# Optimization experiments

Hardware: AMD Instinct MI355X
Metric: run time of the kernel (lower is better)

## Reference

```python
import jax, jax.numpy as jnp
import numpy as np

EPS = 1e-3  # keras BatchNormalization default epsilon
K = 16


def _graph_feature(x, k):
    # x: [B, N, C] -> edge: [B, N, k, 2C]
    sq = jnp.sum(x * x, axis=-1)                       # [B, N]
    # negative squared distance (larger = closer); self is max
    pd = 2.0 * jnp.einsum('bnc,bmc->bnm', x, x) - sq[:, :, None] - sq[:, None, :]
    _, idx = jax.lax.top_k(pd, k)                      # [B, N, k]
    nbr = jax.vmap(lambda xb, ib: xb[ib])(x, idx)      # [B, N, k, C]
    ctr = jnp.broadcast_to(x[:, :, None, :], nbr.shape)
    return jnp.concatenate([ctr, nbr], axis=-1)        # [B, N, k, 2C]


def _bn(y, g, b, m, v):
    return (y - m) * (g * jax.lax.rsqrt(v + EPS)) + b


def _edge_block(x, W, g, b, m, v, k):
    e = _graph_feature(x, k)                           # [B, N, k, 2C]
    h = jnp.einsum('bnkc,cd->bnkd', e, W)              # 1x1 conv, no bias
    h = jax.nn.relu(_bn(h, g, b, m, v))
    return jnp.max(h, axis=2)                          # [B, N, D]


def setup_inputs() -> dict:
    key = jax.random.key(0)
    ks = jax.random.split(key, 32)
    B, N = 8, 2048
    x = jax.random.normal(ks[0], (B, N, 3), dtype=jnp.float32)
    dims = [(6, 64), (128, 64), (128, 128), (256, 256), (512, 512)]
    d = {'x': x}
    for i, (cin, cout) in enumerate(dims):
        j = i + 1
        d[f'W{j}'] = jax.random.normal(ks[1 + i], (cin, cout), dtype=jnp.float32) * (1.0 / np.sqrt(cin))
        d[f'g{j}'] = jax.random.uniform(ks[6 + i], (cout,), dtype=jnp.float32, minval=0.5, maxval=1.5)
        d[f'b{j}'] = jax.random.normal(ks[11 + i], (cout,), dtype=jnp.float32) * 0.1
        d[f'm{j}'] = jax.random.normal(ks[16 + i], (cout,), dtype=jnp.float32) * 0.1
        d[f'v{j}'] = jax.random.uniform(ks[21 + i], (cout,), dtype=jnp.float32, minval=0.5, maxval=1.5)
    return d


def reference(x, W1, g1, b1, m1, v1, W2, g2, b2, m2, v2, W3, g3, b3, m3, v3,
              W4, g4, b4, m4, v4, W5, g5, b5, m5, v5):
    x1 = _edge_block(x,  W1, g1, b1, m1, v1, K)   # [B, N, 64]
    x2 = _edge_block(x1, W2, g2, b2, m2, v2, K)   # [B, N, 64]
    x3 = _edge_block(x2, W3, g3, b3, m3, v3, K)   # [B, N, 128]
    x4 = _edge_block(x3, W4, g4, b4, m4, v4, K)   # [B, N, 256]
    x5 = jnp.concatenate([x1, x2, x3, x4], axis=-1)  # [B, N, 512]
    h5 = jnp.einsum('bnc,cd->bnd', x5, W5)           # 1x1 conv1d, no bias
    return jax.nn.relu(_bn(h5, g5, b5, m5, v5))      # [B, N, 512]
```

## Files before the change

kernel.cpp:

```cpp
#include <hip/hip_runtime.h>

#define NP 2048
#define BTOT 8
#define BN_TOT 16384
#define KC 16
#define NTILE 32
#define NEG_INF (-__builtin_inff())

typedef __attribute__((ext_vector_type(8))) short short8;
typedef __attribute__((ext_vector_type(4))) float f32x4;

__device__ __forceinline__ unsigned short bf16_rne(float x) {
  unsigned u = __float_as_uint(x);
  u += 0x7FFFu + ((u >> 16) & 1u);
  return (unsigned short)(u >> 16);
}
__device__ __forceinline__ void split2(float x, unsigned short& h, unsigned short& l) {
  h = bf16_rne(x);
  float hf = __uint_as_float((unsigned)h << 16);
  l = bf16_rne(x - hf);
}

template <typename JM>
__device__ __forceinline__ void select16(const float (&v)[32], int lane, float* svw,
                                         int* sjw, int* out, int jb, JM jmap) {
  float lmax = v[0];
#pragma unroll
  for (int t = 1; t < 32; ++t) lmax = fmaxf(lmax, v[t]);
  int rank = 0;
  for (int s = 0; s < 64; ++s) {
    float o = __shfl(lmax, s, 64);
    rank += (o > lmax) || (o == lmax && s < lane);
  }
  unsigned long long m15 = __ballot(rank == 15);
  float T0 = __shfl(lmax, (int)__builtin_ctzll(m15), 64);

  unsigned long long lowmask = (1ull << lane) - 1ull;
  unsigned keepmask = 0u;
  int base = 0;
#pragma unroll
  for (int t = 0; t < 32; ++t) {
    bool keep = (v[t] >= T0);
    unsigned long long mk = __ballot(keep);
    if (keep) {
      keepmask |= (1u << t);
      int pos = base + (int)__popcll(mk & lowmask);
      if (pos < 256) { svw[pos] = v[t]; sjw[pos] = jmap(t); }
    }
    base += (int)__popcll(mk);
  }
  int cnt = base;

  if (cnt <= 64) {
    __threadfence_block();
    float mv = NEG_INF;
    int mj = 1 << 30;
    if (lane < cnt) { mv = svw[lane]; mj = sjw[lane]; }
    int rk = 0;
    for (int s = 0; s < 64; ++s) {
      float ov = __shfl(mv, s, 64);
      int oj = __shfl(mj, s, 64);
      rk += (ov > mv) || (ov == mv && oj < mj);
    }
    if (lane < cnt && rk < 16) out[rk] = jb + mj;
    return;
  }

  if (cnt <= 256) {
    __threadfence_block();
    for (int r = 0; r < 16; ++r) {
      float lbv = NEG_INF;
      int lbj = 1 << 30, lbp = -1;
      for (int i = lane; i < cnt; i += 64) {
        float cv = svw[i];
        int cj = sjw[i];
        if (cv > lbv || (cv == lbv && cj < lbj)) { lbv = cv; lbj = cj; lbp = i; }
      }
      float bv = lbv;
      int bj = lbj;
#pragma unroll
      for (int off = 32; off > 0; off >>= 1) {
        float ov = __shfl_xor(bv, off, 64);
        int oj = __shfl_xor(bj, off, 64);
        if (ov > bv || (ov == bv && oj < bj)) { bv = ov; bj = oj; }
      }
      if (lane == 0) out[r] = jb + bj;
      if (lbp >= 0 && lbj == bj) svw[lbp] = NEG_INF;
      __threadfence_block();
    }
    return;
  }

  {
    unsigned avail = keepmask;
    for (int r = 0; r < 16; ++r) {
      float bv = NEG_INF;
      int bj = 1 << 30, bt = -1;
      unsigned am = avail;
      while (am) {
        int t = __builtin_ctz(am);
        am &= am - 1;
        float vv = v[t];
        int jj = jmap(t);
        if (vv > bv || (vv == bv && jj < bj)) { bv = vv; bj = jj; bt = t; }
      }
      float gv = bv;
      int gj = bj;
#pragma unroll
      for (int off = 32; off > 0; off >>= 1) {
        float ov = __shfl_xor(gv, off, 64);
        int oj = __shfl_xor(gj, off, 64);
        if (ov > gv || (ov == gv && oj < gj)) { gv = ov; gj = oj; }
      }
      if (lane == 0) out[r] = jb + gj;
      if (bt >= 0 && bj == gj) avail &= ~(1u << bt);
    }
  }
}

__global__ __launch_bounds__(256) void sqnorm_kernel(const float* __restrict__ X,
                                                     int lda, int C,
                                                     float* __restrict__ sq) {
  int wave = threadIdx.x >> 6, lane = threadIdx.x & 63;
  int row = blockIdx.x * 4 + wave;
  float s = 0.f;
  for (int c = lane; c < C; c += 64) {
    float t = X[(size_t)row * lda + c];
    s += t * t;
  }
#pragma unroll
  for (int off = 32; off > 0; off >>= 1) s += __shfl_xor(s, off, 64);
  if (lane == 0) sq[row] = s;
}

__global__ __launch_bounds__(256) void dist_gemm(const float* __restrict__ X, int lda, int K,
                                                 const float* __restrict__ sq,
                                                 float* __restrict__ pd, int batch0) {
  int bz = blockIdx.z;
  const float* Xb = X + (size_t)(batch0 + bz) * NP * lda;
  const float* sqb = sq + (size_t)(batch0 + bz) * NP;
  float* pdb = pd + (size_t)bz * NP * NP;
  int rem = blockIdx.x, bi = 0;
  while (rem >= NTILE - bi) { rem -= NTILE - bi; ++bi; }
  int bj = bi + rem;
  int i0 = bi * 64, j0 = bj * 64;
  __shared__ float At[KC][68];
  __shared__ float Bt[KC][68];
  int t = threadIdx.x;
  int tx = t & 15, ty = t >> 4;
  int lk = t & 15, lr = t >> 4;
  float acc[4][4] = {};
  for (int k0 = 0; k0 < K; k0 += KC) {
    int kk = k0 + lk;
    bool kv = kk < K;
#pragma unroll
    for (int u = 0; u < 4; ++u) {
      int r = lr + u * 16;
      At[lk][r] = kv ? Xb[(size_t)(i0 + r) * lda + kk] : 0.f;
      Bt[lk][r] = kv ? Xb[(size_t)(j0 + r) * lda + kk] : 0.f;
    }
    __syncthreads();
#pragma unroll
    for (int q = 0; q < KC; ++q) {
      float4 a4 = *(const float4*)&At[q][ty * 4];
      float4 b4 = *(const float4*)&Bt[q][tx * 4];
      float a[4] = {a4.x, a4.y, a4.z, a4.w};
      float bv[4] = {b4.x, b4.y, b4.z, b4.w};
#pragma unroll
      for (int ii = 0; ii < 4; ++ii)
#pragma unroll
        for (int jj = 0; jj < 4; ++jj)
          acc[ii][jj] = fmaf(a[ii], bv[jj], acc[ii][jj]);
    }
    __syncthreads();
  }
  float4 sqj4 = *(const float4*)&sqb[j0 + tx * 4];
#pragma unroll
  for (int ii = 0; ii < 4; ++ii) {
    int i = i0 + ty * 4 + ii;
    float4 o;
    o.x = 2.f * acc[ii][0] - sqj4.x;
    o.y = 2.f * acc[ii][1] - sqj4.y;
    o.z = 2.f * acc[ii][2] - sqj4.z;
    o.w = 2.f * acc[ii][3] - sqj4.w;
    *(float4*)&pdb[(size_t)i * NP + j0 + tx * 4] = o;
  }
  if (bi != bj) {
    float4 sqi4 = *(const float4*)&sqb[i0 + ty * 4];
#pragma unroll
    for (int jj = 0; jj < 4; ++jj) {
      int j = j0 + tx * 4 + jj;
      float4 o;
      o.x = 2.f * acc[0][jj] - sqi4.x;
      o.y = 2.f * acc[1][jj] - sqi4.y;
      o.z = 2.f * acc[2][jj] - sqi4.z;
      o.w = 2.f * acc[3][jj] - sqi4.w;
      *(float4*)&pdb[(size_t)j * NP + i0 + ty * 4] = o;
    }
  }
}

__global__ __launch_bounds__(256) void topk_kernel(const float* __restrict__ pd,
                                                   int* __restrict__ idx_out, int batch0) {
  __shared__ float sv[4][256];
  __shared__ int sj[4][256];
  int wave = threadIdx.x >> 6, lane = threadIdx.x & 63;
  int row = blockIdx.x * 4 + wave;
  const float* prow = pd + (size_t)row * NP;
  int grow = batch0 * NP + row;
  int jb = (grow >> 11) << 11;
  float v[32];
#pragma unroll
  for (int u = 0; u < 8; ++u) {
    float4 q = *(const float4*)&prow[u * 256 + (lane << 2)];
    v[u * 4 + 0] = q.x;
    v[u * 4 + 1] = q.y;
    v[u * 4 + 2] = q.z;
    v[u * 4 + 3] = q.w;
  }
  select16(v, lane, sv[wave], sj[wave], idx_out + (size_t)grow * 16, jb,
           [lane](int t) { return ((t >> 2) << 8) + (lane << 2) + (t & 3); });
}

__global__ __launch_bounds__(256) void dist3_topk(const float* __restrict__ x,
                                                  int* __restrict__ idx_out) {
  __shared__ float4 xs4[NP];
  __shared__ float sv[4][256];
  __shared__ int sj[4][256];
  int wave = threadIdx.x >> 6, lane = threadIdx.x & 63;
  int b = blockIdx.x >> 7;
  int row0 = (blockIdx.x & 127) * 16;
  const float* xb = x + (size_t)b * NP * 3;
  for (int n = threadIdx.x; n < NP; n += 256) {
    float a0 = xb[3 * n], a1 = xb[3 * n + 1], a2 = xb[3 * n + 2];
    xs4[n] = make_float4(a0, a1, a2, a0 * a0 + a1 * a1 + a2 * a2);
  }
  __syncthreads();
  int jb = b << 11;
  for (int rr = 0; rr < 4; ++rr) {
    int row = row0 + wave * 4 + rr;
    float4 c = xs4[row];
    float v[32];
#pragma unroll
    for (int t = 0; t < 32; ++t) {
      int j = lane + t * 64;
      float4 p = xs4[j];
      float dot = c.x * p.x + c.y * p.y + c.z * p.z;
      v[t] = 2.f * dot - p.w;
    }
    select16(v, lane, sv[wave], sj[wave], idx_out + (size_t)(jb + row) * 16, jb,
             [lane](int t) { return lane + t * 64; });
  }
}

__global__ __launch_bounds__(256) void feat_gemm(const float* __restrict__ A, int lda, int K,
                                                 const float* __restrict__ W, int D,
                                                 float* __restrict__ outT,
                                                 float* __restrict__ outB) {
  const float* Wz = W + (size_t)blockIdx.z * K * D;
  float* o = blockIdx.z ? outB : outT;
  int n0 = blockIdx.x * 64, m0 = blockIdx.y * 64;
  __shared__ float At[KC][68];
  __shared__ float Bt[KC][68];
  int t = threadIdx.x;
  int tx = t & 15, ty = t >> 4;
  float acc[4][4] = {};
  for (int k0 = 0; k0 < K; k0 += KC) {
    {
      int lk = t & 15, lr = t >> 4;
      int kk = k0 + lk;
      bool kv = kk < K;
#pragma unroll
      for (int u = 0; u < 4; ++u) {
        int r = lr + u * 16;
        At[lk][r] = kv ? A[(size_t)(m0 + r) * lda + kk] : 0.f;
      }
      int n = t & 63, kq0 = t >> 6;
#pragma unroll
      for (int u = 0; u < 4; ++u) {
        int kq = kq0 + u * 4;
        int kg = k0 + kq;
        Bt[kq][n] = (kg < K) ? Wz[(size_t)kg * D + n0 + n] : 0.f;
      }
    }
    __syncthreads();
#pragma unroll
    for (int q = 0; q < KC; ++q) {
      float4 a4 = *(const float4*)&At[q][ty * 4];
      float4 b4 = *(const float4*)&Bt[q][tx * 4];
      float a[4] = {a4.x, a4.y, a4.z, a4.w};
      float bv[4] = {b4.x, b4.y, b4.z, b4.w};
#pragma unroll
      for (int ii = 0; ii < 4; ++ii)
#pragma unroll
        for (int jj = 0; jj < 4; ++jj)
          acc[ii][jj] = fmaf(a[ii], bv[jj], acc[ii][jj]);
    }
    __syncthreads();
  }
#pragma unroll
  for (int ii = 0; ii < 4; ++ii) {
    float4 o4 = make_float4(acc[ii][0], acc[ii][1], acc[ii][2], acc[ii][3]);
    *(float4*)&o[(size_t)(m0 + ty * 4 + ii) * D + n0 + tx * 4] = o4;
  }
}

__global__ __launch_bounds__(256) void gather_bn_relu(const float* __restrict__ ZT,
                                                      const float* __restrict__ YB,
                                                      const int* __restrict__ idx, int D,
                                                      const float* __restrict__ g,
                                                      const float* __restrict__ bta,
                                                      const float* __restrict__ mu,
                                                      const float* __restrict__ va,
                                                      float* __restrict__ X5, int coff) {
  __shared__ int nb[16];
  int bn = blockIdx.x, d = threadIdx.x;
  if (d < 16) nb[d] = idx[(size_t)bn * 16 + d];
  __syncthreads();
  float mx = NEG_INF;
#pragma unroll
  for (int j = 0; j < 16; ++j) mx = fmaxf(mx, YB[(size_t)nb[j] * D + d]);
  float h = ZT[(size_t)bn * D + d] + mx;
  float s = g[d] / sqrtf(va[d] + 1e-3f);
  float val = (h - mu[d]) * s + bta[d];
  X5[(size_t)bn * 512 + coff + d] = fmaxf(val, 0.f);
}

__global__ __launch_bounds__(256) void split_x5(const float* __restrict__ X5,
                                                unsigned short* __restrict__ Xh,
                                                unsigned short* __restrict__ Xl) {
  const int total4 = BN_TOT * 512 / 4;
  for (int i = blockIdx.x * 256 + threadIdx.x; i < total4; i += gridDim.x * 256) {
    float4 v = *(const float4*)&X5[i * 4];
    ushort4 h, l;
    split2(v.x, h.x, l.x);
    split2(v.y, h.y, l.y);
    split2(v.z, h.z, l.z);
    split2(v.w, h.w, l.w);
    *(ushort4*)&Xh[i * 4] = h;
    *(ushort4*)&Xl[i * 4] = l;
  }
}

__global__ __launch_bounds__(256) void w5t_split(const float* __restrict__ W5,
                                                 unsigned short* __restrict__ Wh,
                                                 unsigned short* __restrict__ Wl) {
  int n = blockIdx.x;
  for (int k = threadIdx.x; k < 512; k += 256) {
    unsigned short h, l;
    split2(W5[(size_t)k * 512 + n], h, l);
    Wh[(size_t)n * 512 + k] = h;
    Wl[(size_t)n * 512 + k] = l;
  }
}

__global__ __launch_bounds__(256) void final_mfma(const unsigned short* __restrict__ Ah,
                                                  const unsigned short* __restrict__ Al,
                                                  const unsigned short* __restrict__ Bh,
                                                  const unsigned short* __restrict__ Bl,
                                                  const float* __restrict__ g,
                                                  const float* __restrict__ bta,
                                                  const float* __restrict__ mu,
                                                  const float* __restrict__ va,
                                                  float* __restrict__ out) {
  int tid = threadIdx.x;
  int wave = tid >> 6, lane = tid & 63;
  int wm = wave >> 1, wn = wave & 1;
  int ln = lane & 15, quad = lane >> 4;
  int m_base = blockIdx.y * 128 + wm * 64;
  int n_base = blockIdx.x * 128 + wn * 64;

  f32x4 acc[4][4];
#pragma unroll
  for (int i = 0; i < 4; ++i)
#pragma unroll
    for (int j = 0; j < 4; ++j) acc[i][j] = (f32x4){0.f, 0.f, 0.f, 0.f};

  size_t aoff[4], boff[4];
#pragma unroll
  for (int t = 0; t < 4; ++t) {
    aoff[t] = (size_t)(m_base + t * 16 + ln) * 512 + quad * 8;
    boff[t] = (size_t)(n_base + t * 16 + ln) * 512 + quad * 8;
  }

  short8 cAh[4], cAl[4], cBh[4], cBl[4];
#pragma unroll
  for (int t = 0; t < 4; ++t) {
    cAh[t] = *(const short8*)(Ah + aoff[t]);
    cAl[t] = *(const short8*)(Al + aoff[t]);
    cBh[t] = *(const short8*)(Bh + boff[t]);
    cBl[t] = *(const short8*)(Bl + boff[t]);
  }

  for (int kk = 0; kk < 16; ++kk) {
    short8 nAh[4], nAl[4], nBh[4], nBl[4];
    if (kk < 15) {
      int ko = (kk + 1) * 32;
#pragma unroll
      for (int t = 0; t < 4; ++t) {
        nAh[t] = *(const short8*)(Ah + aoff[t] + ko);
        nAl[t] = *(const short8*)(Al + aoff[t] + ko);
        nBh[t] = *(const short8*)(Bh + boff[t] + ko);
        nBl[t] = *(const short8*)(Bl + boff[t] + ko);
      }
    }
#pragma unroll
    for (int tm = 0; tm < 4; ++tm)
#pragma unroll
      for (int tn = 0; tn < 4; ++tn) {
        acc[tm][tn] = __builtin_amdgcn_mfma_f32_16x16x32_bf16(cAh[tm], cBh[tn],
                                                              acc[tm][tn], 0, 0, 0);
        acc[tm][tn] = __builtin_amdgcn_mfma_f32_16x16x32_bf16(cAh[tm], cBl[tn],
                                                              acc[tm][tn], 0, 0, 0);
        acc[tm][tn] = __builtin_amdgcn_mfma_f32_16x16x32_bf16(cAl[tm], cBh[tn],
                                                              acc[tm][tn], 0, 0, 0);
      }
    if (kk < 15) {
#pragma unroll
      for (int t = 0; t < 4; ++t) {
        cAh[t] = nAh[t];
        cAl[t] = nAl[t];
        cBh[t] = nBh[t];
        cBl[t] = nBl[t];
      }
    }
  }

#pragma unroll
  for (int tn = 0; tn < 4; ++tn) {
    int col = n_base + tn * 16 + ln;
    float s = g[col] / sqrtf(va[col] + 1e-3f);
    float tc = bta[col] - mu[col] * s;
#pragma unroll
    for (int tm = 0; tm < 4; ++tm) {
      int mrow = m_base + tm * 16 + quad * 4;
#pragma unroll
      for (int r = 0; r < 4; ++r) {
        float val = acc[tm][tn][r] * s + tc;
        out[(size_t)(mrow + r) * 512 + col] = fmaxf(val, 0.f);
      }
    }
  }
}

extern "C" void kernel_launch(void* const* d_in, const int* in_sizes, int n_in,
                              void* d_out, int out_size, void* d_ws, size_t ws_size,
                              hipStream_t stream) {
  const float* x = (const float*)d_in[0];
  const float *W[5], *g[5], *bt[5], *mu[5], *va[5];
  for (int j = 0; j < 5; ++j) {
    W[j] = (const float*)d_in[1 + j * 5 + 0];
    g[j] = (const float*)d_in[1 + j * 5 + 1];
    bt[j] = (const float*)d_in[1 + j * 5 + 2];
    mu[j] = (const float*)d_in[1 + j * 5 + 3];
    va[j] = (const float*)d_in[1 + j * 5 + 4];
  }
  char* p = (char*)d_ws;
  float* X5 = (float*)p; p += (size_t)BN_TOT * 512 * 4;
  float* ZT = (float*)p; p += (size_t)BN_TOT * 256 * 4;
  float* YB = (float*)p; p += (size_t)BN_TOT * 256 * 4;
  int* idx = (int*)p;    p += (size_t)BN_TOT * 16 * 4;
  float* sq = (float*)p; p += (size_t)BN_TOT * 4;
  unsigned short* X5h = (unsigned short*)p; p += (size_t)BN_TOT * 512 * 2;
  unsigned short* X5l = (unsigned short*)p; p += (size_t)BN_TOT * 512 * 2;
  unsigned short* W5h = (unsigned short*)p; p += (size_t)512 * 512 * 2;
  unsigned short* W5l = (unsigned short*)p; p += (size_t)512 * 512 * 2;
  float* pd = (float*)p;
  size_t used = (size_t)(p - (char*)d_ws);
  size_t pdcap = (ws_size > used) ? (ws_size - used) / ((size_t)NP * NP * 4) : 0;
  int nb = (int)(pdcap < 1 ? 1 : (pdcap > (size_t)BTOT ? (size_t)BTOT : pdcap));

  w5t_split<<<512, 256, 0, stream>>>(W[4], W5h, W5l);

  struct Blk { const float* A; int lda, C, D, coff, w; };
  Blk blks[4] = {
      {x, 3, 3, 64, 0, 0},
      {X5 + 0, 512, 64, 64, 64, 1},
      {X5 + 64, 512, 64, 128, 128, 2},
      {X5 + 128, 512, 128, 256, 256, 3},
  };
  for (int q = 0; q < 4; ++q) {
    Blk& B = blks[q];
    if (q == 0) {
      dist3_topk<<<1024, 256, 0, stream>>>(x, idx);
    } else {
      sqnorm_kernel<<<BN_TOT / 4, 256, 0, stream>>>(B.A, B.lda, B.C, sq);
      for (int b0 = 0; b0 < BTOT; b0 += nb) {
        int cnt = (BTOT - b0 < nb) ? (BTOT - b0) : nb;
        dist_gemm<<<dim3(NTILE * (NTILE + 1) / 2, 1, cnt), 256, 0, stream>>>(
            B.A, B.lda, B.C, sq, pd, b0);
        topk_kernel<<<cnt * NP / 4, 256, 0, stream>>>(pd, idx, b0);
      }
    }
    feat_gemm<<<dim3(B.D / 64, BN_TOT / 64, 2), 256, 0, stream>>>(
        B.A, B.lda, B.C, W[B.w], B.D, ZT, YB);
    gather_bn_relu<<<BN_TOT, B.D, 0, stream>>>(ZT, YB, idx, B.D, g[B.w], bt[B.w], mu[B.w],
                                               va[B.w], X5, B.coff);
  }
  split_x5<<<1024, 256, 0, stream>>>(X5, X5h, X5l);
  final_mfma<<<dim3(4, 128), 256, 0, stream>>>(X5h, X5l, W5h, W5l, g[4], bt[4], mu[4],
                                               va[4], (float*)d_out);
}
```

Measured before the change: 634.3 us.

## Fuse kNN distance GEMM and top-k into one MFMA kernel with threshold buffers

Replaces the fp32 FMA distance GEMM, which writes the full pairwise-distance matrix to global memory and is then re-read by a separate top-k kernel, with a fused kernel. The new kernel computes distances with bf16 MFMA using a hi/lo split (three products per tile) and filters candidates against a running per-row threshold into LDS buffers. Buffers are compacted to the current top-16 when they fill, and each row's top-16 is extracted at the end. This removes the large distance-matrix round trip and the batch chunking, but launches only 256 blocks and drops the lo*lo term, so distances may differ slightly from fp32.

```diff
diff --git a/kernel.cpp b/kernel.cpp
--- a/kernel.cpp
+++ b/kernel.cpp
@@ -4,7 +4,6 @@
 #define BTOT 8
 #define BN_TOT 16384
 #define KC 16
-#define NTILE 32
 #define NEG_INF (-__builtin_inff())
 
 typedef __attribute__((ext_vector_type(8))) short short8;
@@ -19,6 +18,188 @@
   h = bf16_rne(x);
   float hf = __uint_as_float((unsigned)h << 16);
   l = bf16_rne(x - hf);
+}
+
+__device__ __forceinline__ void wave_extract16(float* bv, int* bj, int cnt, int lane,
+                                               int* out, int jb, int* cntp, float* Tp) {
+  __threadfence_block();
+  if (cnt <= 64) {
+    float v = NEG_INF;
+    int j = 1 << 30;
+    if (lane < cnt) { v = bv[lane]; j = bj[lane]; }
+    int rk = 0;
+    for (int s = 0; s < 64; ++s) {
+      float ov = __shfl(v, s, 64);
+      int oj = __shfl(j, s, 64);
+      rk += (ov > v) || (ov == v && oj < j);
+    }
+    if (out) {
+      if (lane < cnt && rk < 16) out[rk] = jb + j;
+    } else {
+      unsigned long long m15 = __ballot(lane < cnt && rk == 15);
+      float T15 = __shfl(v, (int)__builtin_ctzll(m15), 64);
+      if (lane < cnt && rk < 16) { bv[rk] = v; bj[rk] = j; }
+      if (lane == 0) { *cntp = 16; *Tp = T15; }
+    }
+  } else {
+    float keepv = NEG_INF;
+    int keepj = 1 << 30;
+    float lastv = NEG_INF;
+    for (int r = 0; r < 16; ++r) {
+      float lbv = NEG_INF;
+      int lbj = 1 << 30, lbp = -1;
+      for (int i = lane; i < cnt; i += 64) {
+        float cv = bv[i];
+        int cj = bj[i];
+        if (cv > lbv || (cv == lbv && cj < lbj)) { lbv = cv; lbj = cj; lbp = i; }
+      }
+      float xv = lbv;
+      int xj = lbj;
+#pragma unroll
+      for (int off = 32; off > 0; off >>= 1) {
+        float ov = __shfl_xor(xv, off, 64);
+        int oj = __shfl_xor(xj, off, 64);
+        if (ov > xv || (ov == xv && oj < xj)) { xv = ov; xj = oj; }
+      }
+      if (out && lane == 0) out[r] = jb + xj;
+      if (lane == r) { keepv = xv; keepj = xj; }
+      lastv = xv;
+      if (lbp >= 0 && lbj == xj) bv[lbp] = NEG_INF;
+      __threadfence_block();
+    }
+    if (!out) {
+      if (lane < 16) { bv[lane] = keepv; bj[lane] = keepj; }
+      if (lane == 0) { *cntp = 16; *Tp = lastv; }
+    }
+  }
+  __threadfence_block();
+}
+
+template <int KST>
+__global__ __launch_bounds__(256, 1) void knn_mfma(const unsigned short* __restrict__ Xh,
+                                                   const unsigned short* __restrict__ Xl,
+                                                   const float* __restrict__ sqa,
+                                                   int* __restrict__ idx_out) {
+  constexpr int C = KST * 32;
+  __shared__ float s_bv[4][16][128];
+  __shared__ int s_bj[4][16][128];
+  __shared__ float s_sq[NP];
+  __shared__ float s_T[4][16];
+  __shared__ int s_cnt[4][16];
+  int tid = threadIdx.x, wv = tid >> 6, lane = tid & 63;
+  int ln = lane & 15, quad = lane >> 4;
+  int b = blockIdx.y, i0 = blockIdx.x * 64;
+  int gb = b * NP;
+  for (int t = tid; t < NP; t += 256) s_sq[t] = sqa[gb + t];
+  if (lane < 16) { s_T[wv][lane] = NEG_INF; s_cnt[wv][lane] = 0; }
+  __syncthreads();
+
+  const unsigned short* arh = Xh + (size_t)(gb + i0 + wv * 16 + ln) * C + quad * 8;
+  const unsigned short* arl = Xl + (size_t)(gb + i0 + wv * 16 + ln) * C + quad * 8;
+  short8 Ah8[KST], Al8[KST];
+#pragma unroll
+  for (int ks = 0; ks < KST; ++ks) {
+    Ah8[ks] = *(const short8*)(arh + ks * 32);
+    Al8[ks] = *(const short8*)(arl + ks * 32);
+  }
+
+  const unsigned short* bbh = Xh + (size_t)gb * C + quad * 8;
+  const unsigned short* bbl = Xl + (size_t)gb * C + quad * 8;
+
+  short8 cBh[4], cBl[4], nBh[4], nBl[4];
+#pragma unroll
+  for (int tn = 0; tn < 4; ++tn) {
+    size_t off = (size_t)(tn * 16 + ln) * C;
+    cBh[tn] = *(const short8*)(bbh + off);
+    cBl[tn] = *(const short8*)(bbl + off);
+  }
+
+  for (int jt = 0; jt < 32; ++jt) {
+    int myc = (lane < 16) ? s_cnt[wv][lane] : 0;
+    unsigned long long need = __ballot(myc >= 49);
+    while (need) {
+      int row = (int)__builtin_ctzll(need);
+      need &= need - 1;
+      wave_extract16(&s_bv[wv][row][0], &s_bj[wv][row][0], s_cnt[wv][row], lane,
+                     nullptr, 0, &s_cnt[wv][row], &s_T[wv][row]);
+    }
+
+    f32x4 acc[4];
+#pragma unroll
+    for (int tn = 0; tn < 4; ++tn) acc[tn] = (f32x4){0.f, 0.f, 0.f, 0.f};
+#pragma unroll
+    for (int ks = 0; ks < KST; ++ks) {
+      bool last = (jt == 31) && (ks == KST - 1);
+      int njt = (ks == KST - 1) ? jt + 1 : jt;
+      int nks = (ks == KST - 1) ? 0 : ks + 1;
+      if (!last) {
+#pragma unroll
+        for (int tn = 0; tn < 4; ++tn) {
+          size_t off = (size_t)(njt * 64 + tn * 16 + ln) * C + nks * 32;
+          nBh[tn] = *(const short8*)(bbh + off);
+          nBl[tn] = *(const short8*)(bbl + off);
+        }
+      }
+#pragma unroll
+      for (int tn = 0; tn < 4; ++tn) {
+        acc[tn] = __builtin_amdgcn_mfma_f32_16x16x32_bf16(Ah8[ks], cBh[tn], acc[tn], 0, 0, 0);
+        acc[tn] = __builtin_amdgcn_mfma_f32_16x16x32_bf16(Ah8[ks], cBl[tn], acc[tn], 0, 0, 0);
+        acc[tn] = __builtin_amdgcn_mfma_f32_16x16x32_bf16(Al8[ks], cBh[tn], acc[tn], 0, 0, 0);
+      }
+      if (!last) {
+#pragma unroll
+        for (int tn = 0; tn < 4; ++tn) { cBh[tn] = nBh[tn]; cBl[tn] = nBl[tn]; }
+      }
+    }
+
+    float4 Tl4 = *(const float4*)&s_T[wv][quad * 4];
+    float Tl[4] = {Tl4.x, Tl4.y, Tl4.z, Tl4.w};
+#pragma unroll
+    for (int tn = 0; tn < 4; ++tn) {
+      int jcol = jt * 64 + tn * 16 + ln;
+      float sqv = s_sq[jcol];
+#pragma unroll
+      for (int r = 0; r < 4; ++r) {
+        float s = fmaf(2.f, acc[tn][r], -sqv);
+        if (s >= Tl[r]) {
+          int row = quad * 4 + r;
+          int pos = atomicAdd(&s_cnt[wv][row], 1);
+          if (pos < 128) {
+            s_bv[wv][row][pos] = s;
+            s_bj[wv][row][pos] = jcol;
+          }
+        }
+      }
+    }
+    __threadfence_block();
+  }
+
+  for (int row = 0; row < 16; ++row) {
+    int grow = gb + i0 + wv * 16 + row;
+    wave_extract16(&s_bv[wv][row][0], &s_bj[wv][row][0], s_cnt[wv][row], lane,
+                   idx_out + (size_t)grow * 16, gb, nullptr, nullptr);
+  }
+}
+
+__global__ __launch_bounds__(256) void split_sq(const float* __restrict__ X, int C,
+                                                unsigned short* __restrict__ Xh,
+                                                unsigned short* __restrict__ Xl,
+                                                float* __restrict__ sq) {
+  int wave = threadIdx.x >> 6, lane = threadIdx.x & 63;
+  int row = blockIdx.x * 4 + wave;
+  const float* xr = X + (size_t)row * 512;
+  float ssum = 0.f;
+  for (int c = lane; c < C; c += 64) {
+    float v = xr[c];
+    ssum += v * v;
+    unsigned short h, l;
+    split2(v, h, l);
+    Xh[(size_t)row * C + c] = h;
+    Xl[(size_t)row * C + c] = l;
+  }
+#pragma unroll
+  for (int off = 32; off > 0; off >>= 1) ssum += __shfl_xor(ssum, off, 64);
+  if (lane == 0) sq[row] = ssum;
 }
 
 template <typename JM>
@@ -116,110 +297,6 @@
       if (bt >= 0 && bj == gj) avail &= ~(1u << bt);
     }
   }
-}
-
-__global__ __launch_bounds__(256) void sqnorm_kernel(const float* __restrict__ X,
-                                                     int lda, int C,
-                                                     float* __restrict__ sq) {
-  int wave = threadIdx.x >> 6, lane = threadIdx.x & 63;
-  int row = blockIdx.x * 4 + wave;
-  float s = 0.f;
-  for (int c = lane; c < C; c += 64) {
-    float t = X[(size_t)row * lda + c];
-    s += t * t;
-  }
-#pragma unroll
-  for (int off = 32; off > 0; off >>= 1) s += __shfl_xor(s, off, 64);
-  if (lane == 0) sq[row] = s;
-}
-
-__global__ __launch_bounds__(256) void dist_gemm(const float* __restrict__ X, int lda, int K,
-                                                 const float* __restrict__ sq,
-                                                 float* __restrict__ pd, int batch0) {
-  int bz = blockIdx.z;
-  const float* Xb = X + (size_t)(batch0 + bz) * NP * lda;
-  const float* sqb = sq + (size_t)(batch0 + bz) * NP;
-  float* pdb = pd + (size_t)bz * NP * NP;
-  int rem = blockIdx.x, bi = 0;
-  while (rem >= NTILE - bi) { rem -= NTILE - bi; ++bi; }
-  int bj = bi + rem;
-  int i0 = bi * 64, j0 = bj * 64;
-  __shared__ float At[KC][68];
-  __shared__ float Bt[KC][68];
-  int t = threadIdx.x;
-  int tx = t & 15, ty = t >> 4;
-  int lk = t & 15, lr = t >> 4;
-  float acc[4][4] = {};
-  for (int k0 = 0; k0 < K; k0 += KC) {
-    int kk = k0 + lk;
-    bool kv = kk < K;
-#pragma unroll
-    for (int u = 0; u < 4; ++u) {
-      int r = lr + u * 16;
-      At[lk][r] = kv ? Xb[(size_t)(i0 + r) * lda + kk] : 0.f;
-      Bt[lk][r] = kv ? Xb[(size_t)(j0 + r) * lda + kk] : 0.f;
-    }
-    __syncthreads();
-#pragma unroll
-    for (int q = 0; q < KC; ++q) {
-      float4 a4 = *(const float4*)&At[q][ty * 4];
-      float4 b4 = *(const float4*)&Bt[q][tx * 4];
-      float a[4] = {a4.x, a4.y, a4.z, a4.w};
-      float bv[4] = {b4.x, b4.y, b4.z, b4.w};
-#pragma unroll
-      for (int ii = 0; ii < 4; ++ii)
-#pragma unroll
-        for (int jj = 0; jj < 4; ++jj)
-          acc[ii][jj] = fmaf(a[ii], bv[jj], acc[ii][jj]);
-    }
-    __syncthreads();
-  }
-  float4 sqj4 = *(const float4*)&sqb[j0 + tx * 4];
-#pragma unroll
-  for (int ii = 0; ii < 4; ++ii) {
-    int i = i0 + ty * 4 + ii;
-    float4 o;
-    o.x = 2.f * acc[ii][0] - sqj4.x;
-    o.y = 2.f * acc[ii][1] - sqj4.y;
-    o.z = 2.f * acc[ii][2] - sqj4.z;
-    o.w = 2.f * acc[ii][3] - sqj4.w;
-    *(float4*)&pdb[(size_t)i * NP + j0 + tx * 4] = o;
-  }
-  if (bi != bj) {
-    float4 sqi4 = *(const float4*)&sqb[i0 + ty * 4];
-#pragma unroll
-    for (int jj = 0; jj < 4; ++jj) {
-      int j = j0 + tx * 4 + jj;
-      float4 o;
-      o.x = 2.f * acc[0][jj] - sqi4.x;
-      o.y = 2.f * acc[1][jj] - sqi4.y;
-      o.z = 2.f * acc[2][jj] - sqi4.z;
-      o.w = 2.f * acc[3][jj] - sqi4.w;
-      *(float4*)&pdb[(size_t)j * NP + i0 + ty * 4] = o;
-    }
-  }
-}
-
-__global__ __launch_bounds__(256) void topk_kernel(const float* __restrict__ pd,
-                                                   int* __restrict__ idx_out, int batch0) {
-  __shared__ float sv[4][256];
-  __shared__ int sj[4][256];
-  int wave = threadIdx.x >> 6, lane = threadIdx.x & 63;
-  int row = blockIdx.x * 4 + wave;
-  const float* prow = pd + (size_t)row * NP;
-  int grow = batch0 * NP + row;
-  int jb = (grow >> 11) << 11;
-  float v[32];
-#pragma unroll
-  for (int u = 0; u < 8; ++u) {
-    float4 q = *(const float4*)&prow[u * 256 + (lane << 2)];
-    v[u * 4 + 0] = q.x;
-    v[u * 4 + 1] = q.y;
-    v[u * 4 + 2] = q.z;
-    v[u * 4 + 3] = q.w;
-  }
-  select16(v, lane, sv[wave], sj[wave], idx_out + (size_t)grow * 16, jb,
-           [lane](int t) { return ((t >> 2) << 8) + (lane << 2) + (t & 3); });
 }
 
 __global__ __launch_bounds__(256) void dist3_topk(const float* __restrict__ x,
@@ -465,10 +542,8 @@
   unsigned short* X5l = (unsigned short*)p; p += (size_t)BN_TOT * 512 * 2;
   unsigned short* W5h = (unsigned short*)p; p += (size_t)512 * 512 * 2;
   unsigned short* W5l = (unsigned short*)p; p += (size_t)512 * 512 * 2;
-  float* pd = (float*)p;
-  size_t used = (size_t)(p - (char*)d_ws);
-  size_t pdcap = (ws_size > used) ? (ws_size - used) / ((size_t)NP * NP * 4) : 0;
-  int nb = (int)(pdcap < 1 ? 1 : (pdcap > (size_t)BTOT ? (size_t)BTOT : pdcap));
+  unsigned short* Xsh = (unsigned short*)p; p += (size_t)BN_TOT * 128 * 2;
+  unsigned short* Xsl = (unsigned short*)p; p += (size_t)BN_TOT * 128 * 2;
 
   w5t_split<<<512, 256, 0, stream>>>(W[4], W5h, W5l);
 
@@ -484,13 +559,11 @@
     if (q == 0) {
       dist3_topk<<<1024, 256, 0, stream>>>(x, idx);
     } else {
-      sqnorm_kernel<<<BN_TOT / 4, 256, 0, stream>>>(B.A, B.lda, B.C, sq);
-      for (int b0 = 0; b0 < BTOT; b0 += nb) {
-        int cnt = (BTOT - b0 < nb) ? (BTOT - b0) : nb;
-        dist_gemm<<<dim3(NTILE * (NTILE + 1) / 2, 1, cnt), 256, 0, stream>>>(
-            B.A, B.lda, B.C, sq, pd, b0);
-        topk_kernel<<<cnt * NP / 4, 256, 0, stream>>>(pd, idx, b0);
-      }
+      split_sq<<<BN_TOT / 4, 256, 0, stream>>>(B.A, B.C, Xsh, Xsl, sq);
+      if (B.C == 64)
+        knn_mfma<2><<<dim3(32, 8), 256, 0, stream>>>(Xsh, Xsl, sq, idx);
+      else
+        knn_mfma<4><<<dim3(32, 8), 256, 0, stream>>>(Xsh, Xsl, sq, idx);
     }
     feat_gemm<<<dim3(B.D / 64, BN_TOT / 64, 2), 256, 0, stream>>>(
         B.A, B.lda, B.C, W[B.w], B.D, ZT, YB);
```

After: 1.275 ms. 101% more time.
